# Performance work log

Measured on AMD Instinct MI355X. Metric: run time of the kernel, lower is better.

The kernel has to match this reference:

```python
import jax, jax.numpy as jnp
import numpy as np

H = 512   # hidden_size
V = 128   # vec_size / output_size
L = 8192  # sequence length


def _gru_cell(x, h, Wih, Whh, bih, bhh):
    # torch GRU cell: gates ordered (r, z, n)
    gx = x @ Wih.T + bih            # [3H]
    gh = h @ Whh.T + bhh            # [3H]
    xr, xz, xn = jnp.split(gx, 3)
    hr, hz, hn = jnp.split(gh, 3)
    r = jax.nn.sigmoid(xr + hr)
    z = jax.nn.sigmoid(xz + hz)
    n = jnp.tanh(xn + r * hn)
    return (1.0 - z) * n + z * h


def _run_gru2(xs, h0, h1, p0, p1):
    """2-layer GRU over xs [L, in]; returns ((h0_f, h1_f), top-layer outputs [L, H])."""
    def step(carry, x):
        c0, c1 = carry
        c0 = _gru_cell(x, c0, *p0)
        c1 = _gru_cell(c0, c1, *p1)
        return (c0, c1), c1
    return jax.lax.scan(step, (h0, h1), xs)


def setup_inputs() -> dict:
    key = jax.random.key(0)
    ks = jax.random.split(key, 24)
    b = 1.0 / np.sqrt(H)  # torch default uniform init bound
    u = lambda k, shape: jax.random.uniform(k, shape, jnp.float32, -b, b)
    inp = {
        "src": jax.random.normal(ks[0], (L, V), jnp.float32),
        "trg": jax.random.uniform(ks[1], (L, V), jnp.float32),
        # encoder GRU (input V -> hidden H, 2 layers)
        "enc_Wih0": u(ks[2], (3 * H, V)),  "enc_Whh0": u(ks[3], (3 * H, H)),
        "enc_bih0": u(ks[4], (3 * H,)),    "enc_bhh0": u(ks[5], (3 * H,)),
        "enc_Wih1": u(ks[6], (3 * H, H)),  "enc_Whh1": u(ks[7], (3 * H, H)),
        "enc_bih1": u(ks[8], (3 * H,)),    "enc_bhh1": u(ks[9], (3 * H,)),
        # decoder GRU (input V -> hidden H, 2 layers)
        "dec_Wih0": u(ks[10], (3 * H, V)), "dec_Whh0": u(ks[11], (3 * H, H)),
        "dec_bih0": u(ks[12], (3 * H,)),   "dec_bhh0": u(ks[13], (3 * H,)),
        "dec_Wih1": u(ks[14], (3 * H, H)), "dec_Whh1": u(ks[15], (3 * H, H)),
        "dec_bih1": u(ks[16], (3 * H,)),   "dec_bhh1": u(ks[17], (3 * H,)),
        # output projection
        "Wout": u(ks[18], (V, H)), "bout": u(ks[19], (V,)),
    }
    return inp


def reference(src, trg,
              enc_Wih0, enc_Whh0, enc_bih0, enc_bhh0,
              enc_Wih1, enc_Whh1, enc_bih1, enc_bhh1,
              dec_Wih0, dec_Whh0, dec_bih0, dec_bhh0,
              dec_Wih1, dec_Whh1, dec_bih1, dec_bhh1,
              Wout, bout):
    z = jnp.zeros((H,), src.dtype)
    # Encoder: run 2-layer GRU over src, keep final per-layer states
    (h0, h1), _ = _run_gru2(
        src, z, z,
        (enc_Wih0, enc_Whh0, enc_bih0, enc_bhh0),
        (enc_Wih1, enc_Whh1, enc_bih1, enc_bhh1))
    # Decoder inputs under full teacher forcing: trg[0], trg[0], trg[1], ... trg[L-2]
    dec_in = jax.nn.relu(jnp.concatenate([trg[:1], trg[:-1]], axis=0))  # [L, V]
    _, ys = _run_gru2(
        dec_in, h0, h1,
        (dec_Wih0, dec_Whh0, dec_bih0, dec_bhh0),
        (dec_Wih1, dec_Whh1, dec_bih1, dec_bhh1))  # ys: [L, H] top-layer outputs
    outputs = jax.nn.sigmoid(ys @ Wout.T + bout)   # [L, V]
    return outputs
```

## Files before the change

kernel.cpp:

```cpp
#include <hip/hip_runtime.h>

#define Hh   512
#define Vv   128
#define LL   8192
#define G3   1536
#define NBK  256
#define NPAIR 1024

#define OFF_GX   0ull
#define OFF_YS   50331648ull
#define OFF_RECE 67108864ull
#define OFF_RECD (OFF_RECE + 16384ull)
#define OFF_WT   (OFF_RECD + 16384ull)

__device__ __forceinline__ float sigm(float x)  { return 1.f / (1.f + __expf(-x)); }
__device__ __forceinline__ float tanha(float x) { return 2.f / (1.f + __expf(-2.f * x)) - 1.f; }

__device__ __forceinline__ unsigned long long packpair(float v, int t) {
    return ((unsigned long long)(unsigned)t << 32) | (unsigned long long)__float_as_uint(v);
}
__device__ __forceinline__ int   pair_tag(unsigned long long p) { return (int)(p >> 32); }
__device__ __forceinline__ float pair_val(unsigned long long p) { return __uint_as_float((unsigned)p); }

template <int CTRL>
__device__ __forceinline__ float dpp_add(float m) {
    int t = __builtin_amdgcn_update_dpp(0, __builtin_bit_cast(int, m), CTRL, 0xF, 0xF, true);
    return m + __builtin_bit_cast(float, t);
}

__global__ __launch_bounds__(256) void gemm_gx(
    const float* __restrict__ X, const float* __restrict__ Wih,
    const float* __restrict__ bih, float* __restrict__ gxo, int shift_relu)
{
    __shared__ float xs[16][128];
    const int tid = threadIdx.x;
    const int m0  = blockIdx.x * 16;
    const int c   = blockIdx.y * 256 + tid;

    for (int i = tid; i < 16 * 128; i += 256) {
        const int r = i >> 7, k = i & 127;
        int srow = m0 + r;
        if (shift_relu) srow = (srow == 0) ? 0 : (srow - 1);
        float v = X[(size_t)srow * Vv + k];
        if (shift_relu) v = fmaxf(v, 0.f);
        xs[r][k] = v;
    }
    __syncthreads();

    const float4* wp = (const float4*)(Wih + (size_t)c * Vv);
    float4 wr[32];
#pragma unroll
    for (int q = 0; q < 32; ++q) wr[q] = wp[q];
    const float bb = bih[c];

    for (int m = 0; m < 16; ++m) {
        const float4* xp = (const float4*)xs[m];
        float acc = bb;
#pragma unroll
        for (int q = 0; q < 32; ++q) {
            const float4 x4 = xp[q];
            acc = fmaf(wr[q].x, x4.x, acc); acc = fmaf(wr[q].y, x4.y, acc);
            acc = fmaf(wr[q].z, x4.z, acc); acc = fmaf(wr[q].w, x4.w, acc);
        }
        gxo[(size_t)(m0 + m) * G3 + c] = acc;
    }
}

__global__ __launch_bounds__(64, 1) void seq2(
    const float* __restrict__ gx,
    const float* __restrict__ Whh0, const float* __restrict__ Wih1,
    const float* __restrict__ Whh1,
    const float* __restrict__ bhh0, const float* __restrict__ bih1,
    const float* __restrict__ bhh1,
    unsigned long long* __restrict__ rec,
    float* __restrict__ ys)
{
    const int bid  = blockIdx.x, lane = threadIdx.x;
    const int e0   = 2 * bid;

    int off[8];
#pragma unroll
    for (int j = 0; j < 8; ++j) off[j] = (e0 + lane + 64 * j) & 511;

    float wv[18][8];
#pragma unroll
    for (int m = 0; m < 3; ++m) {
        const float* mat = (m == 0) ? Whh0 : (m == 1) ? Wih1 : Whh1;
#pragma unroll
        for (int g = 0; g < 3; ++g)
#pragma unroll
            for (int i = 0; i < 2; ++i) {
                const float* row = mat + (size_t)(g * Hh + e0 + i) * Hh;
#pragma unroll
                for (int j = 0; j < 8; ++j) wv[m * 6 + g * 2 + i][j] = row[off[j]];
            }
    }
#pragma unroll
    for (int r = 0; r < 18; ++r)
#pragma unroll
        for (int j = 0; j < 8; ++j)
            asm volatile("" : "+a"(wv[r][j]));

    float b_r = 0.f, b_z = 0.f, b_n1 = 0.f, b_n2 = 0.f;
    if (lane < 2) {
        const int e = e0 + lane;
        b_r = bhh0[e]; b_z = bhh0[Hh + e]; b_n1 = bhh0[2 * Hh + e];
    } else if (lane < 4) {
        const int e = e0 + (lane & 1);
        b_r  = bih1[e] + bhh1[e];
        b_z  = bih1[Hh + e] + bhh1[Hh + e];
        b_n1 = bih1[2 * Hh + e];
        b_n2 = bhh1[2 * Hh + e];
    }

    for (int tau = 0; tau <= LL; ++tau) {
        float xr = 0.f, xz = 0.f, xn = 0.f;
        if (lane < 2 && tau < LL) {
            const size_t gb = (size_t)tau * G3 + e0 + lane;
            xr = gx[gb]; xz = gx[gb + Hh]; xn = gx[gb + 2 * Hh];
        }

        const int need = tau - 1;
        const unsigned long long* rp = rec + (size_t)((tau - 1) & 1) * NPAIR;
        unsigned long long p0[8], p1[8];
        int ok;
        do {
#pragma unroll
            for (int j = 0; j < 8; ++j)
                p0[j] = __hip_atomic_load(rp + off[j],      __ATOMIC_RELAXED, __HIP_MEMORY_SCOPE_AGENT);
#pragma unroll
            for (int j = 0; j < 8; ++j)
                p1[j] = __hip_atomic_load(rp + Hh + off[j], __ATOMIC_RELAXED, __HIP_MEMORY_SCOPE_AGENT);
            ok = 1;
#pragma unroll
            for (int j = 0; j < 8; ++j)
                ok &= (pair_tag(p0[j]) >= need) & (pair_tag(p1[j]) >= need);
        } while (!__all(ok));

        float h0v[8], h1v[8];
#pragma unroll
        for (int j = 0; j < 8; ++j) { h0v[j] = pair_val(p0[j]); h1v[j] = pair_val(p1[j]); }

#pragma unroll
        for (int r = 0; r < 18; ++r)
#pragma unroll
            for (int j = 0; j < 8; ++j)
                asm volatile("" : "+a"(wv[r][j]));

        float acc[18];
#pragma unroll
        for (int r = 0; r < 18; ++r) acc[r] = 0.f;
#pragma unroll
        for (int j = 0; j < 8; ++j) {
#pragma unroll
            for (int r = 0; r < 12; ++r) acc[r] = fmaf(wv[r][j], h0v[j], acc[r]);
#pragma unroll
            for (int r = 12; r < 18; ++r) acc[r] = fmaf(wv[r][j], h1v[j], acc[r]);
        }

        float sred[9];
#pragma unroll
        for (int k = 0; k < 9; ++k) {
            float a = dpp_add<0xB1>(acc[2 * k]);
            float c = dpp_add<0xB1>(acc[2 * k + 1]);
            float m = (lane & 1) ? c : a;
            m = dpp_add<0x122>(m);
            m = dpp_add<0x124>(m);
            m = dpp_add<0x128>(m);
            m += __shfl_xor(m, 16);
            m += __shfl_xor(m, 32);
            sred[k] = m;
        }

        const float h1p = __shfl(h1v[0], lane & 1);

        unsigned long long* recw = rec + (size_t)(tau & 1) * NPAIR;
        if (lane < 2) {
            if (tau < LL) {
                const float rg = sigm(xr + sred[0] + b_r);
                const float zg = sigm(xz + sred[1] + b_z);
                const float ng = tanha(xn + rg * (sred[2] + b_n1));
                const float hnew = (1.f - zg) * ng + zg * h0v[0];
                __hip_atomic_store(recw + e0 + lane, packpair(hnew, tau),
                                   __ATOMIC_RELAXED, __HIP_MEMORY_SCOPE_AGENT);
            }
        } else if (lane < 4) {
            const int e = e0 + (lane & 1);
            float hnew;
            if (tau >= 1) {
                const float rg = sigm(sred[3] + sred[6] + b_r);
                const float zg = sigm(sred[4] + sred[7] + b_z);
                const float ng = tanha(sred[5] + b_n1 + rg * (sred[8] + b_n2));
                hnew = (1.f - zg) * ng + zg * h1p;
                if (ys) ys[(size_t)(tau - 1) * Hh + e] = hnew;
            } else {
                hnew = h1p;
            }
            __hip_atomic_store(recw + Hh + e, packpair(hnew, tau),
                               __ATOMIC_RELAXED, __HIP_MEMORY_SCOPE_AGENT);
        }
    }
}

__global__ __launch_bounds__(256) void transposeW(const float* __restrict__ W,
                                                  float* __restrict__ WT,
                                                  unsigned long long* __restrict__ encr)
{
    const int i = blockIdx.x * 256 + threadIdx.x;
    WT[(i & 511) * 128 + (i >> 9)] = W[i];
    if (i < NPAIR) {
        __hip_atomic_store(encr + NPAIR + i, packpair(0.f, -1),
                           __ATOMIC_RELAXED, __HIP_MEMORY_SCOPE_AGENT);
        __hip_atomic_store(encr + i, packpair(0.f, -2),
                           __ATOMIC_RELAXED, __HIP_MEMORY_SCOPE_AGENT);
    }
}

__global__ __launch_bounds__(256) void handoff(const unsigned long long* __restrict__ encr,
                                               unsigned long long* __restrict__ decr)
{
    const int p = blockIdx.x * 256 + threadIdx.x;
    const unsigned long long src = __hip_atomic_load(
        encr + (p < Hh ? NPAIR : 0) + p, __ATOMIC_RELAXED, __HIP_MEMORY_SCOPE_AGENT);
    __hip_atomic_store(decr + NPAIR + p, packpair(pair_val(src), -1),
                       __ATOMIC_RELAXED, __HIP_MEMORY_SCOPE_AGENT);
    __hip_atomic_store(decr + p, packpair(0.f, -2),
                       __ATOMIC_RELAXED, __HIP_MEMORY_SCOPE_AGENT);
}

__global__ __launch_bounds__(128) void out_proj(
    const float* __restrict__ ys, const float* __restrict__ WT,
    const float* __restrict__ bout, float* __restrict__ out)
{
    __shared__ float yss[16][512];
    const int tid = threadIdx.x;
    const int m0  = blockIdx.x * 16;

    for (int i = tid; i < 16 * 512; i += 128)
        yss[i >> 9][i & 511] = ys[(size_t)(m0 + (i >> 9)) * 512 + (i & 511)];
    __syncthreads();

    const int c = tid;
    float acc[16];
    const float b = bout[c];
#pragma unroll
    for (int m = 0; m < 16; ++m) acc[m] = b;

    for (int k4 = 0; k4 < 128; ++k4) {
        const float w0 = WT[(4 * k4 + 0) * 128 + c];
        const float w1 = WT[(4 * k4 + 1) * 128 + c];
        const float w2 = WT[(4 * k4 + 2) * 128 + c];
        const float w3 = WT[(4 * k4 + 3) * 128 + c];
#pragma unroll
        for (int m = 0; m < 16; ++m) {
            const float4 yv = *(const float4*)&yss[m][4 * k4];
            acc[m] = fmaf(w0, yv.x, fmaf(w1, yv.y, fmaf(w2, yv.z, fmaf(w3, yv.w, acc[m]))));
        }
    }
#pragma unroll
    for (int m = 0; m < 16; ++m)
        out[(size_t)(m0 + m) * 128 + c] = 1.f / (1.f + __expf(-acc[m]));
}

extern "C" void kernel_launch(void* const* d_in, const int* in_sizes, int n_in,
                              void* d_out, int out_size, void* d_ws, size_t ws_size,
                              hipStream_t stream)
{
    const float* src      = (const float*)d_in[0];
    const float* trg      = (const float*)d_in[1];
    const float* eWih0    = (const float*)d_in[2];
    const float* eWhh0    = (const float*)d_in[3];
    const float* ebih0    = (const float*)d_in[4];
    const float* ebhh0    = (const float*)d_in[5];
    const float* eWih1    = (const float*)d_in[6];
    const float* eWhh1    = (const float*)d_in[7];
    const float* ebih1    = (const float*)d_in[8];
    const float* ebhh1    = (const float*)d_in[9];
    const float* dWih0    = (const float*)d_in[10];
    const float* dWhh0    = (const float*)d_in[11];
    const float* dbih0    = (const float*)d_in[12];
    const float* dbhh0    = (const float*)d_in[13];
    const float* dWih1    = (const float*)d_in[14];
    const float* dWhh1    = (const float*)d_in[15];
    const float* dbih1    = (const float*)d_in[16];
    const float* dbhh1    = (const float*)d_in[17];
    const float* Wout     = (const float*)d_in[18];
    const float* bout     = (const float*)d_in[19];

    char* ws = (char*)d_ws;
    float*              gx   = (float*)(ws + OFF_GX);
    float*              ys   = (float*)(ws + OFF_YS);
    unsigned long long* recE = (unsigned long long*)(ws + OFF_RECE);
    unsigned long long* recD = (unsigned long long*)(ws + OFF_RECD);
    float*              WT   = (float*)(ws + OFF_WT);

    hipLaunchKernelGGL(transposeW, dim3(256), dim3(256), 0, stream, Wout, WT, recE);

    hipLaunchKernelGGL(gemm_gx, dim3(LL / 16, 6), dim3(256), 0, stream,
                       src, eWih0, ebih0, gx, 0);
    hipLaunchKernelGGL(seq2, dim3(NBK), dim3(64), 0, stream,
                       gx, eWhh0, eWih1, eWhh1, ebhh0, ebih1, ebhh1,
                       recE, (float*)nullptr);

    hipLaunchKernelGGL(handoff, dim3(4), dim3(256), 0, stream, recE, recD);
    hipLaunchKernelGGL(gemm_gx, dim3(LL / 16, 6), dim3(256), 0, stream,
                       trg, dWih0, dbih0, gx, 1);
    hipLaunchKernelGGL(seq2, dim3(NBK), dim3(64), 0, stream,
                       gx, dWhh0, dWih1, dWhh1, dbhh0, dbih1, dbhh1,
                       recD, ys);

    hipLaunchKernelGGL(out_proj, dim3(LL / 16), dim3(128), 0, stream,
                       ys, WT, bout, (float*)d_out);

    (void)in_sizes; (void)n_in; (void)out_size; (void)ws_size;
}
```

Measured before the change: 35.64 ms.

## Replicate recurrent state buffers eight ways and prefetch next-step gate inputs

Measured after the change: 34.29 ms. -3.8%, faster.

```diff
diff --git a/kernel.cpp b/kernel.cpp
--- a/kernel.cpp
+++ b/kernel.cpp
@@ -6,12 +6,14 @@
 #define G3   1536
 #define NBK  256
 #define NPAIR 1024
+#define NREP 8
+#define RSTR (2*NPAIR)
 
 #define OFF_GX   0ull
 #define OFF_YS   50331648ull
 #define OFF_RECE 67108864ull
-#define OFF_RECD (OFF_RECE + 16384ull)
-#define OFF_WT   (OFF_RECD + 16384ull)
+#define OFF_RECD (OFF_RECE + 131072ull)
+#define OFF_WT   (OFF_RECD + 131072ull)
 
 __device__ __forceinline__ float sigm(float x)  { return 1.f / (1.f + __expf(-x)); }
 __device__ __forceinline__ float tanha(float x) { return 2.f / (1.f + __expf(-2.f * x)) - 1.f; }
@@ -77,6 +79,7 @@
 {
     const int bid  = blockIdx.x, lane = threadIdx.x;
     const int e0   = 2 * bid;
+    const unsigned long long* myrep = rec + (size_t)(bid & 7) * RSTR;
 
     int off[8];
 #pragma unroll
@@ -113,15 +116,15 @@
         b_n2 = bhh1[2 * Hh + e];
     }
 
+    float xr = 0.f, xz = 0.f, xn = 0.f;
+    if (lane < 2) {
+        const size_t gb = (size_t)0 * G3 + e0 + lane;
+        xr = gx[gb]; xz = gx[gb + Hh]; xn = gx[gb + 2 * Hh];
+    }
+
     for (int tau = 0; tau <= LL; ++tau) {
-        float xr = 0.f, xz = 0.f, xn = 0.f;
-        if (lane < 2 && tau < LL) {
-            const size_t gb = (size_t)tau * G3 + e0 + lane;
-            xr = gx[gb]; xz = gx[gb + Hh]; xn = gx[gb + 2 * Hh];
-        }
-
         const int need = tau - 1;
-        const unsigned long long* rp = rec + (size_t)((tau - 1) & 1) * NPAIR;
+        const unsigned long long* rp = myrep + (size_t)((tau - 1) & 1) * NPAIR;
         unsigned long long p0[8], p1[8];
         int ok;
         do {
@@ -136,6 +139,12 @@
             for (int j = 0; j < 8; ++j)
                 ok &= (pair_tag(p0[j]) >= need) & (pair_tag(p1[j]) >= need);
         } while (!__all(ok));
+
+        float nxr = 0.f, nxz = 0.f, nxn = 0.f;
+        if (lane < 2 && tau + 1 < LL) {
+            const size_t gb = (size_t)(tau + 1) * G3 + e0 + lane;
+            nxr = gx[gb]; nxz = gx[gb + Hh]; nxn = gx[gb + 2 * Hh];
+        }
 
         float h0v[8], h1v[8];
 #pragma unroll
@@ -174,15 +183,19 @@
 
         const float h1p = __shfl(h1v[0], lane & 1);
 
-        unsigned long long* recw = rec + (size_t)(tau & 1) * NPAIR;
+        const size_t slotoff = (size_t)(tau & 1) * NPAIR;
         if (lane < 2) {
             if (tau < LL) {
                 const float rg = sigm(xr + sred[0] + b_r);
                 const float zg = sigm(xz + sred[1] + b_z);
                 const float ng = tanha(xn + rg * (sred[2] + b_n1));
                 const float hnew = (1.f - zg) * ng + zg * h0v[0];
-                __hip_atomic_store(recw + e0 + lane, packpair(hnew, tau),
-                                   __ATOMIC_RELAXED, __HIP_MEMORY_SCOPE_AGENT);
+                const unsigned long long pk = packpair(hnew, tau);
+                unsigned long long* w = rec + slotoff + e0 + lane;
+#pragma unroll
+                for (int r = 0; r < NREP; ++r)
+                    __hip_atomic_store(w + (size_t)r * RSTR, pk,
+                                       __ATOMIC_RELAXED, __HIP_MEMORY_SCOPE_AGENT);
             }
         } else if (lane < 4) {
             const int e = e0 + (lane & 1);
@@ -196,9 +209,15 @@
             } else {
                 hnew = h1p;
             }
-            __hip_atomic_store(recw + Hh + e, packpair(hnew, tau),
-                               __ATOMIC_RELAXED, __HIP_MEMORY_SCOPE_AGENT);
-        }
+            const unsigned long long pk = packpair(hnew, tau);
+            unsigned long long* w = rec + slotoff + Hh + e;
+#pragma unroll
+            for (int r = 0; r < NREP; ++r)
+                __hip_atomic_store(w + (size_t)r * RSTR, pk,
+                                   __ATOMIC_RELAXED, __HIP_MEMORY_SCOPE_AGENT);
+        }
+
+        xr = nxr; xz = nxz; xn = nxn;
     }
 }
 
@@ -209,10 +228,13 @@
     const int i = blockIdx.x * 256 + threadIdx.x;
     WT[(i & 511) * 128 + (i >> 9)] = W[i];
     if (i < NPAIR) {
-        __hip_atomic_store(encr + NPAIR + i, packpair(0.f, -1),
-                           __ATOMIC_RELAXED, __HIP_MEMORY_SCOPE_AGENT);
-        __hip_atomic_store(encr + i, packpair(0.f, -2),
-                           __ATOMIC_RELAXED, __HIP_MEMORY_SCOPE_AGENT);
+#pragma unroll
+        for (int r = 0; r < NREP; ++r) {
+            __hip_atomic_store(encr + (size_t)r * RSTR + NPAIR + i, packpair(0.f, -1),
+                               __ATOMIC_RELAXED, __HIP_MEMORY_SCOPE_AGENT);
+            __hip_atomic_store(encr + (size_t)r * RSTR + i, packpair(0.f, -2),
+                               __ATOMIC_RELAXED, __HIP_MEMORY_SCOPE_AGENT);
+        }
     }
 }
 
@@ -222,10 +244,13 @@
     const int p = blockIdx.x * 256 + threadIdx.x;
     const unsigned long long src = __hip_atomic_load(
         encr + (p < Hh ? NPAIR : 0) + p, __ATOMIC_RELAXED, __HIP_MEMORY_SCOPE_AGENT);
-    __hip_atomic_store(decr + NPAIR + p, packpair(pair_val(src), -1),
-                       __ATOMIC_RELAXED, __HIP_MEMORY_SCOPE_AGENT);
-    __hip_atomic_store(decr + p, packpair(0.f, -2),
-                       __ATOMIC_RELAXED, __HIP_MEMORY_SCOPE_AGENT);
+#pragma unroll
+    for (int r = 0; r < NREP; ++r) {
+        __hip_atomic_store(decr + (size_t)r * RSTR + NPAIR + p, packpair(pair_val(src), -1),
+                           __ATOMIC_RELAXED, __HIP_MEMORY_SCOPE_AGENT);
+        __hip_atomic_store(decr + (size_t)r * RSTR + p, packpair(0.f, -2),
+                           __ATOMIC_RELAXED, __HIP_MEMORY_SCOPE_AGENT);
+    }
 }
 
 __global__ __launch_bounds__(128) void out_proj(
```

## Split GRU layers onto separate block groups with ring-buffered state handoff

Applied to the files above, without the earlier changes.

Result: faster. 32.26 ms (median of 2 runs) (-9.5%).

```diff
diff --git a/kernel.cpp b/kernel.cpp
--- a/kernel.cpp
+++ b/kernel.cpp
@@ -5,13 +5,17 @@
 #define LL   8192
 #define G3   1536
 #define NBK  256
-#define NPAIR 1024
-
+#define S0   16
+#define S1   4
+
+#define RECBYTES ((S0*512 + S1*512) * 8ull)
 #define OFF_GX   0ull
 #define OFF_YS   50331648ull
 #define OFF_RECE 67108864ull
-#define OFF_RECD (OFF_RECE + 16384ull)
-#define OFF_WT   (OFF_RECD + 16384ull)
+#define OFF_RECD (OFF_RECE + RECBYTES)
+#define OFF_WT   (OFF_RECD + RECBYTES)
+
+#define H1OFF (S0*512)
 
 __device__ __forceinline__ float sigm(float x)  { return 1.f / (1.f + __expf(-x)); }
 __device__ __forceinline__ float tanha(float x) { return 2.f / (1.f + __expf(-2.f * x)) - 1.f; }
@@ -26,6 +30,17 @@
 __device__ __forceinline__ float dpp_add(float m) {
     int t = __builtin_amdgcn_update_dpp(0, __builtin_bit_cast(int, m), CTRL, 0xF, 0xF, true);
     return m + __builtin_bit_cast(float, t);
+}
+__device__ __forceinline__ float red2(float a, float c, int lane) {
+    a = dpp_add<0xB1>(a);
+    c = dpp_add<0xB1>(c);
+    float m = (lane & 1) ? c : a;
+    m = dpp_add<0x122>(m);
+    m = dpp_add<0x124>(m);
+    m = dpp_add<0x128>(m);
+    m += __shfl_xor(m, 16);
+    m += __shfl_xor(m, 32);
+    return m;
 }
 
 __global__ __launch_bounds__(256) void gemm_gx(
@@ -75,129 +90,180 @@
     unsigned long long* __restrict__ rec,
     float* __restrict__ ys)
 {
-    const int bid  = blockIdx.x, lane = threadIdx.x;
-    const int e0   = 2 * bid;
-
-    int off[8];
-#pragma unroll
-    for (int j = 0; j < 8; ++j) off[j] = (e0 + lane + 64 * j) & 511;
-
-    float wv[18][8];
-#pragma unroll
-    for (int m = 0; m < 3; ++m) {
-        const float* mat = (m == 0) ? Whh0 : (m == 1) ? Wih1 : Whh1;
+    const int bid = blockIdx.x, lane = threadIdx.x;
+    unsigned long long* h0rec = rec;
+    unsigned long long* h1rec = rec + H1OFF;
+
+    if (bid < 128) {
+        const int e0 = 4 * bid;
+        int off[8];
+#pragma unroll
+        for (int j = 0; j < 8; ++j) off[j] = (e0 + lane + 64 * j) & 511;
+
+        float w[12][8];
 #pragma unroll
         for (int g = 0; g < 3; ++g)
 #pragma unroll
-            for (int i = 0; i < 2; ++i) {
-                const float* row = mat + (size_t)(g * Hh + e0 + i) * Hh;
-#pragma unroll
-                for (int j = 0; j < 8; ++j) wv[m * 6 + g * 2 + i][j] = row[off[j]];
-            }
-    }
-#pragma unroll
-    for (int r = 0; r < 18; ++r)
-#pragma unroll
-        for (int j = 0; j < 8; ++j)
-            asm volatile("" : "+a"(wv[r][j]));
-
-    float b_r = 0.f, b_z = 0.f, b_n1 = 0.f, b_n2 = 0.f;
-    if (lane < 2) {
-        const int e = e0 + lane;
-        b_r = bhh0[e]; b_z = bhh0[Hh + e]; b_n1 = bhh0[2 * Hh + e];
-    } else if (lane < 4) {
-        const int e = e0 + (lane & 1);
-        b_r  = bih1[e] + bhh1[e];
-        b_z  = bih1[Hh + e] + bhh1[Hh + e];
-        b_n1 = bih1[2 * Hh + e];
-        b_n2 = bhh1[2 * Hh + e];
-    }
-
-    for (int tau = 0; tau <= LL; ++tau) {
+            for (int i = 0; i < 4; ++i) {
+                const float* row = Whh0 + (size_t)(g * Hh + e0 + i) * Hh;
+#pragma unroll
+                for (int j = 0; j < 8; ++j) w[g * 4 + i][j] = row[off[j]];
+            }
+
+        float b_r = 0.f, b_z = 0.f, b_n = 0.f;
+        if (lane < 4) {
+            const int e = e0 + lane;
+            b_r = bhh0[e]; b_z = bhh0[Hh + e]; b_n = bhh0[2 * Hh + e];
+        }
         float xr = 0.f, xz = 0.f, xn = 0.f;
-        if (lane < 2 && tau < LL) {
-            const size_t gb = (size_t)tau * G3 + e0 + lane;
-            xr = gx[gb]; xz = gx[gb + Hh]; xn = gx[gb + 2 * Hh];
-        }
-
-        const int need = tau - 1;
-        const unsigned long long* rp = rec + (size_t)((tau - 1) & 1) * NPAIR;
-        unsigned long long p0[8], p1[8];
-        int ok;
-        do {
+        if (lane < 4) {
+            xr = gx[e0 + lane]; xz = gx[Hh + e0 + lane]; xn = gx[2 * Hh + e0 + lane];
+        }
+
+        for (int t = 0; t < LL; ++t) {
+            const int need = t - 1;
+            const unsigned long long* rp = h0rec + (size_t)((t + S0 - 1) & (S0 - 1)) * 512;
+            unsigned long long p[8];
+            int ok;
+            do {
+#pragma unroll
+                for (int j = 0; j < 8; ++j)
+                    p[j] = __hip_atomic_load(rp + off[j], __ATOMIC_RELAXED, __HIP_MEMORY_SCOPE_AGENT);
+                ok = 1;
+#pragma unroll
+                for (int j = 0; j < 8; ++j) ok &= (pair_tag(p[j]) >= need);
+            } while (!__all(ok));
+
+            if ((t & 7) == 0) {
+                const int gneed = t - 4;
+                const unsigned long long* gp = h1rec + (size_t)(t & (S1 - 1)) * 512;
+                int gok;
+                do {
+                    gok = 1;
+#pragma unroll
+                    for (int j = 0; j < 8; ++j) {
+                        const unsigned long long q = __hip_atomic_load(
+                            gp + ((lane + 64 * j) & 511), __ATOMIC_RELAXED, __HIP_MEMORY_SCOPE_AGENT);
+                        gok &= (pair_tag(q) >= gneed);
+                    }
+                } while (!__all(gok));
+            }
+
+            float nxr = 0.f, nxz = 0.f, nxn = 0.f;
+            if (lane < 4 && t + 1 < LL) {
+                const size_t gb = (size_t)(t + 1) * G3 + e0 + lane;
+                nxr = gx[gb]; nxz = gx[gb + Hh]; nxn = gx[gb + 2 * Hh];
+            }
+
+            float h0v[8];
+#pragma unroll
+            for (int j = 0; j < 8; ++j) h0v[j] = pair_val(p[j]);
+
+            float acc[12];
+#pragma unroll
+            for (int r = 0; r < 12; ++r) acc[r] = 0.f;
 #pragma unroll
             for (int j = 0; j < 8; ++j)
-                p0[j] = __hip_atomic_load(rp + off[j],      __ATOMIC_RELAXED, __HIP_MEMORY_SCOPE_AGENT);
-#pragma unroll
-            for (int j = 0; j < 8; ++j)
-                p1[j] = __hip_atomic_load(rp + Hh + off[j], __ATOMIC_RELAXED, __HIP_MEMORY_SCOPE_AGENT);
-            ok = 1;
-#pragma unroll
-            for (int j = 0; j < 8; ++j)
-                ok &= (pair_tag(p0[j]) >= need) & (pair_tag(p1[j]) >= need);
-        } while (!__all(ok));
-
-        float h0v[8], h1v[8];
-#pragma unroll
-        for (int j = 0; j < 8; ++j) { h0v[j] = pair_val(p0[j]); h1v[j] = pair_val(p1[j]); }
-
-#pragma unroll
-        for (int r = 0; r < 18; ++r)
-#pragma unroll
-            for (int j = 0; j < 8; ++j)
-                asm volatile("" : "+a"(wv[r][j]));
-
-        float acc[18];
-#pragma unroll
-        for (int r = 0; r < 18; ++r) acc[r] = 0.f;
-#pragma unroll
-        for (int j = 0; j < 8; ++j) {
-#pragma unroll
-            for (int r = 0; r < 12; ++r) acc[r] = fmaf(wv[r][j], h0v[j], acc[r]);
-#pragma unroll
-            for (int r = 12; r < 18; ++r) acc[r] = fmaf(wv[r][j], h1v[j], acc[r]);
-        }
-
-        float sred[9];
-#pragma unroll
-        for (int k = 0; k < 9; ++k) {
-            float a = dpp_add<0xB1>(acc[2 * k]);
-            float c = dpp_add<0xB1>(acc[2 * k + 1]);
-            float m = (lane & 1) ? c : a;
-            m = dpp_add<0x122>(m);
-            m = dpp_add<0x124>(m);
-            m = dpp_add<0x128>(m);
-            m += __shfl_xor(m, 16);
-            m += __shfl_xor(m, 32);
-            sred[k] = m;
-        }
-
-        const float h1p = __shfl(h1v[0], lane & 1);
-
-        unsigned long long* recw = rec + (size_t)(tau & 1) * NPAIR;
-        if (lane < 2) {
-            if (tau < LL) {
-                const float rg = sigm(xr + sred[0] + b_r);
-                const float zg = sigm(xz + sred[1] + b_z);
-                const float ng = tanha(xn + rg * (sred[2] + b_n1));
+#pragma unroll
+                for (int r = 0; r < 12; ++r) acc[r] = fmaf(w[r][j], h0v[j], acc[r]);
+
+            float sred[6];
+#pragma unroll
+            for (int k = 0; k < 6; ++k) sred[k] = red2(acc[2 * k], acc[2 * k + 1], lane);
+
+            if (lane < 4) {
+                const int i2 = lane >> 1;
+                const float rg = sigm(xr + sred[i2] + b_r);
+                const float zg = sigm(xz + sred[2 + i2] + b_z);
+                const float ng = tanha(xn + rg * (sred[4 + i2] + b_n));
                 const float hnew = (1.f - zg) * ng + zg * h0v[0];
-                __hip_atomic_store(recw + e0 + lane, packpair(hnew, tau),
-                                   __ATOMIC_RELAXED, __HIP_MEMORY_SCOPE_AGENT);
-            }
-        } else if (lane < 4) {
-            const int e = e0 + (lane & 1);
-            float hnew;
-            if (tau >= 1) {
-                const float rg = sigm(sred[3] + sred[6] + b_r);
-                const float zg = sigm(sred[4] + sred[7] + b_z);
-                const float ng = tanha(sred[5] + b_n1 + rg * (sred[8] + b_n2));
-                hnew = (1.f - zg) * ng + zg * h1p;
-                if (ys) ys[(size_t)(tau - 1) * Hh + e] = hnew;
-            } else {
-                hnew = h1p;
-            }
-            __hip_atomic_store(recw + Hh + e, packpair(hnew, tau),
-                               __ATOMIC_RELAXED, __HIP_MEMORY_SCOPE_AGENT);
+                __hip_atomic_store(h0rec + (size_t)(t & (S0 - 1)) * 512 + e0 + lane,
+                                   packpair(hnew, t), __ATOMIC_RELAXED, __HIP_MEMORY_SCOPE_AGENT);
+            }
+            xr = nxr; xz = nxz; xn = nxn;
+        }
+    } else {
+        const int e0 = 4 * (bid - 128);
+        int off[8];
+#pragma unroll
+        for (int j = 0; j < 8; ++j) off[j] = (e0 + lane + 64 * j) & 511;
+
+        float wA[12][8], wB[12][8];
+#pragma unroll
+        for (int g = 0; g < 3; ++g)
+#pragma unroll
+            for (int i = 0; i < 4; ++i) {
+                const float* rowA = Wih1 + (size_t)(g * Hh + e0 + i) * Hh;
+                const float* rowB = Whh1 + (size_t)(g * Hh + e0 + i) * Hh;
+#pragma unroll
+                for (int j = 0; j < 8; ++j) {
+                    wA[g * 4 + i][j] = rowA[off[j]];
+                    wB[g * 4 + i][j] = rowB[off[j]];
+                }
+            }
+
+        float b_r = 0.f, b_z = 0.f, b_n1 = 0.f, b_n2 = 0.f;
+        if (lane < 4) {
+            const int e = e0 + lane;
+            b_r  = bih1[e] + bhh1[e];
+            b_z  = bih1[Hh + e] + bhh1[Hh + e];
+            b_n1 = bih1[2 * Hh + e];
+            b_n2 = bhh1[2 * Hh + e];
+        }
+
+        for (int t = 0; t < LL; ++t) {
+            const unsigned long long* rp0 = h0rec + (size_t)(t & (S0 - 1)) * 512;
+            const unsigned long long* rp1 = h1rec + (size_t)((t + S1 - 1) & (S1 - 1)) * 512;
+            unsigned long long p0[8], p1[8];
+            int ok;
+            do {
+#pragma unroll
+                for (int j = 0; j < 8; ++j)
+                    p0[j] = __hip_atomic_load(rp0 + off[j], __ATOMIC_RELAXED, __HIP_MEMORY_SCOPE_AGENT);
+#pragma unroll
+                for (int j = 0; j < 8; ++j)
+                    p1[j] = __hip_atomic_load(rp1 + off[j], __ATOMIC_RELAXED, __HIP_MEMORY_SCOPE_AGENT);
+                ok = 1;
+#pragma unroll
+                for (int j = 0; j < 8; ++j)
+                    ok &= (pair_tag(p0[j]) >= t) & (pair_tag(p1[j]) >= t - 1);
+            } while (!__all(ok));
+
+            float h0v[8], h1v[8];
+#pragma unroll
+            for (int j = 0; j < 8; ++j) { h0v[j] = pair_val(p0[j]); h1v[j] = pair_val(p1[j]); }
+
+            float acc[16];
+#pragma unroll
+            for (int r = 0; r < 16; ++r) acc[r] = 0.f;
+#pragma unroll
+            for (int j = 0; j < 8; ++j) {
+#pragma unroll
+                for (int r = 0; r < 8; ++r) {
+                    acc[r] = fmaf(wA[r][j], h0v[j], acc[r]);
+                    acc[r] = fmaf(wB[r][j], h1v[j], acc[r]);
+                }
+#pragma unroll
+                for (int i = 0; i < 4; ++i) {
+                    acc[8 + i]  = fmaf(wA[8 + i][j], h0v[j], acc[8 + i]);
+                    acc[12 + i] = fmaf(wB[8 + i][j], h1v[j], acc[12 + i]);
+                }
+            }
+
+            float sred[8];
+#pragma unroll
+            for (int k = 0; k < 8; ++k) sred[k] = red2(acc[2 * k], acc[2 * k + 1], lane);
+
+            if (lane < 4) {
+                const int i2 = lane >> 1;
+                const float rg = sigm(sred[i2] + b_r);
+                const float zg = sigm(sred[2 + i2] + b_z);
+                const float ng = tanha(sred[4 + i2] + b_n1 + rg * (sred[6 + i2] + b_n2));
+                const float hnew = (1.f - zg) * ng + zg * h1v[0];
+                if (ys) ys[(size_t)t * Hh + e0 + lane] = hnew;
+                __hip_atomic_store(h1rec + (size_t)(t & (S1 - 1)) * 512 + e0 + lane,
+                                   packpair(hnew, t), __ATOMIC_RELAXED, __HIP_MEMORY_SCOPE_AGENT);
+            }
         }
     }
 }
@@ -208,10 +274,14 @@
 {
     const int i = blockIdx.x * 256 + threadIdx.x;
     WT[(i & 511) * 128 + (i >> 9)] = W[i];
-    if (i < NPAIR) {
-        __hip_atomic_store(encr + NPAIR + i, packpair(0.f, -1),
+    if (i < S0 * 512) {
+        const int slot = i >> 9;
+        __hip_atomic_store(encr + i, packpair(0.f, (slot == S0 - 1) ? -1 : -100),
                            __ATOMIC_RELAXED, __HIP_MEMORY_SCOPE_AGENT);
-        __hip_atomic_store(encr + i, packpair(0.f, -2),
+    }
+    if (i < S1 * 512) {
+        const int slot = i >> 9;
+        __hip_atomic_store(encr + H1OFF + i, packpair(0.f, (slot == S1 - 1) ? -1 : slot - 4),
                            __ATOMIC_RELAXED, __HIP_MEMORY_SCOPE_AGENT);
     }
 }
@@ -220,12 +290,30 @@
                                                unsigned long long* __restrict__ decr)
 {
     const int p = blockIdx.x * 256 + threadIdx.x;
-    const unsigned long long src = __hip_atomic_load(
-        encr + (p < Hh ? NPAIR : 0) + p, __ATOMIC_RELAXED, __HIP_MEMORY_SCOPE_AGENT);
-    __hip_atomic_store(decr + NPAIR + p, packpair(pair_val(src), -1),
-                       __ATOMIC_RELAXED, __HIP_MEMORY_SCOPE_AGENT);
-    __hip_atomic_store(decr + p, packpair(0.f, -2),
-                       __ATOMIC_RELAXED, __HIP_MEMORY_SCOPE_AGENT);
+    {
+        const int slot = p >> 9;
+        unsigned long long v;
+        if (slot == S0 - 1) {
+            const unsigned long long src = __hip_atomic_load(
+                encr + p, __ATOMIC_RELAXED, __HIP_MEMORY_SCOPE_AGENT);
+            v = packpair(pair_val(src), -1);
+        } else {
+            v = packpair(0.f, -100);
+        }
+        __hip_atomic_store(decr + p, v, __ATOMIC_RELAXED, __HIP_MEMORY_SCOPE_AGENT);
+    }
+    if (p < S1 * 512) {
+        const int slot = p >> 9;
+        unsigned long long v;
+        if (slot == S1 - 1) {
+            const unsigned long long src = __hip_atomic_load(
+                encr + H1OFF + p, __ATOMIC_RELAXED, __HIP_MEMORY_SCOPE_AGENT);
+            v = packpair(pair_val(src), -1);
+        } else {
+            v = packpair(0.f, slot - 4);
+        }
+        __hip_atomic_store(decr + H1OFF + p, v, __ATOMIC_RELAXED, __HIP_MEMORY_SCOPE_AGENT);
+    }
 }
 
 __global__ __launch_bounds__(128) void out_proj(
@@ -302,7 +390,7 @@
                        gx, eWhh0, eWih1, eWhh1, ebhh0, ebih1, ebhh1,
                        recE, (float*)nullptr);
 
-    hipLaunchKernelGGL(handoff, dim3(4), dim3(256), 0, stream, recE, recD);
+    hipLaunchKernelGGL(handoff, dim3(32), dim3(256), 0, stream, recE, recD);
     hipLaunchKernelGGL(gemm_gx, dim3(LL / 16, 6), dim3(256), 0, stream,
                        trg, dWih0, dbih0, gx, 1);
     hipLaunchKernelGGL(seq2, dim3(NBK), dim3(64), 0, stream,
```
